# Optimization experiments

Hardware: AMD Instinct MI355X
Metric: run time of the kernel (lower is better)

## Reference

```python
import jax, jax.numpy as jnp
import numpy as np

EPS = 1e-10
BLOCK = 8


def _block_rfft2(x):
    # x: (N, 1, H, W) -> real/imag coeffs (N, K, 8, 5), matching torch.rfft(signal_ndim=2)/b**2
    N, C, H, W = x.shape
    b = BLOCK
    Hb, Wb = H // b, W // b
    # non-overlapping 8x8 blocks, row-major over (Hb, Wb) like nn.Unfold with stride=blocksize
    blocks = x[:, 0].reshape(N, Hb, b, Wb, b).transpose(0, 1, 3, 2, 4).reshape(N, Hb * Wb, b, b)
    c = jnp.fft.rfft2(blocks) / (b * b)  # (N, K, 8, 5) complex
    return jnp.real(c).astype(x.dtype), jnp.imag(c).astype(x.dtype)


def _soft_combine(a, b):
    # softmax-weighted blend of a and b along a virtual last axis (factor=1)
    stacked = jnp.stack([a, b], axis=-1)
    f = jax.nn.softmax(stacked, axis=-1)
    return a * f[..., 0] + b * f[..., 1]


def setup_inputs() -> dict:
    key = jax.random.key(0)
    k1, k2 = jax.random.split(key)
    N, H, W = 64, 512, 512
    inp = {
        "input": jax.random.normal(k1, (N, 1, H, W), dtype=jnp.float32),
        "target": jax.random.normal(k2, (N, 1, H, W), dtype=jnp.float32),
        # learned parameters at their init values (weight_size = (8, 5))
        "t_tild": jnp.zeros((BLOCK, BLOCK // 2 + 1), dtype=jnp.float32),
        "alpha": jnp.float32(0.1),
        "w_tild": jnp.float32(np.log(0.2 / 0.8)),
        "beta": jnp.float32(1.0),
        "w_phase_tild": jnp.zeros((BLOCK, BLOCK // 2 + 1), dtype=jnp.float32) - 2.0,
    }
    return inp


def reference(input, target, t_tild, alpha, w_tild, beta, w_phase_tild):
    # blockwise 2D rFFT of both images
    c0r, c0i = _block_rfft2(target)  # (N, K, 8, 5)
    c1r, c1i = _block_rfft2(input)

    # amplitude: frobenius norm over (real, imag) after +EPS, as in torch.norm(c0+EPS, dim=4)
    c0_amp = jnp.sqrt((c0r + EPS) ** 2 + (c0i + EPS) ** 2)
    c1_amp = jnp.sqrt((c1r + EPS) ** 2 + (c1i + EPS) ** 2)

    avg_lum = jnp.mean(c0_amp[:, :, 0, 0])
    t = jnp.exp(t_tild)  # (8, 5)
    lum = ((c0_amp[:, :, 0, 0] + EPS) / (avg_lum + EPS)) ** alpha  # (N, K)
    t_l = t[None, None, :, :] * lum[:, :, None, None]  # (N, K, 8, 5)

    w = jax.nn.sigmoid(w_tild)
    s = _soft_combine(t_l, (jnp.abs(c0_amp) + EPS) ** w * t_l ** (1 - w))

    # Watson amplitude distance (dropout in eval mode = identity)
    watson = (jnp.abs((c0_amp - c1_amp) / s) + EPS) ** beta + EPS
    watson = jnp.sum(watson, axis=(1, 2, 3)) ** (1.0 / beta)  # (N,)

    # phase distance
    c0_phase = jnp.arctan2(c0i, c0r + EPS)
    c1_phase = jnp.arctan2(c1i, c1r + EPS)
    w_phase = jnp.exp(w_phase_tild)  # trainable=True branch: no corner zeroing
    phase_dist = jnp.arccos(jnp.cos(c0_phase - c1_phase) * (1 - EPS * 1e3)) * w_phase
    phase_dist = jnp.sum(phase_dist, axis=(1, 2, 3))  # (N,)

    return watson + phase_dist  # reduction='none' -> (N,)
```

## Files before the change

kernel.cpp:

```cpp
#include <hip/hip_runtime.h>
#include <math.h>

#define EPSf 1e-10f
#define IMG_N 64
#define IMG_H 512
#define IMG_W 512
#define KBLK 4096
#define TOTAL_BLK (IMG_N * KBLK)
#define WG 256
#define NWG (TOTAL_BLK / WG)
#define NWG2 (TOTAL_BLK * 2 / WG)
#define CHUNKS 32

#define KCc 0.70710678118654752440f
#define SCc (1.0f / 64.0f)
#define LOG2E 1.44269504088896340736f

#define FSQRT(x) __builtin_amdgcn_sqrtf(x)
#define FRCP(x)  __builtin_amdgcn_rcpf(x)

__device__ __forceinline__ float dpp_xor1(float x) {
    int i = __builtin_bit_cast(int, x);
    i = __builtin_amdgcn_mov_dpp(i, 0xB1, 0xF, 0xF, true);
    return __builtin_bit_cast(float, i);
}

__device__ __forceinline__ float wave_red(float v) {
#pragma unroll
    for (int o = 32; o > 0; o >>= 1) v += __shfl_down(v, o, 64);
    return v;
}

__global__ __launch_bounds__(WG) void kA(const float* __restrict__ tgt,
                                         float* __restrict__ partA) {
    int gid = blockIdx.x * WG + threadIdx.x;
    int n = gid >> 12;
    int k = gid & 4095;
    int bi = k >> 6, bj = k & 63;
    const float* p = tgt + (size_t)n * (IMG_H * IMG_W) + (size_t)(bi * 8) * IMG_W + bj * 8;
    float s = 0.f;
#pragma unroll
    for (int r = 0; r < 8; r++) {
        float4 a = *(const float4*)(p + (size_t)r * IMG_W);
        float4 b = *(const float4*)(p + (size_t)r * IMG_W + 4);
        s += ((a.x + a.y) + (a.z + a.w)) + ((b.x + b.y) + (b.z + b.w));
    }
    float dc = s * (1.0f / 64.0f);
    float amp = sqrtf((dc + EPSf) * (dc + EPSf) + EPSf * EPSf);
    float wv = wave_red(amp);
    __shared__ float red[4];
    if ((threadIdx.x & 63) == 0) red[threadIdx.x >> 6] = wv;
    __syncthreads();
    if (threadIdx.x == 0) partA[blockIdx.x] = (red[0] + red[1]) + (red[2] + red[3]);
}

__global__ __launch_bounds__(1024) void kB(const float* __restrict__ partA,
                                           float* __restrict__ avgOut) {
    float v = partA[threadIdx.x];
    float wv = wave_red(v);
    __shared__ float red[16];
    if ((threadIdx.x & 63) == 0) red[threadIdx.x >> 6] = wv;
    __syncthreads();
    if (threadIdx.x == 0) {
        float s = 0.f;
#pragma unroll
        for (int i = 0; i < 16; i++) s += red[i];
        avgOut[0] = s * (1.0f / (float)TOTAL_BLK);
    }
}

#define ROWFFT(A, B, P) do { \
    float s02 = (A).x + (B).x, d02 = (A).x - (B).x; \
    float s26 = (A).z + (B).z, d26 = (A).z - (B).z; \
    float s13 = (A).y + (B).y, d13 = (A).y - (B).y; \
    float s37 = (A).w + (B).w, d37 = (A).w - (B).w; \
    float e0 = s02 + s26, e2 = s02 - s26; \
    float o0 = s13 + s37, o2 = s13 - s37; \
    float cp = KCc * (d13 - d37), cm = KCc * (d13 + d37); \
    P##_0 = SCc * (e0 + o0);  P##_1 = SCc * (d02 + cp); \
    P##_2 = SCc * (-d26 - cm); P##_3 = SCc * e2; \
    P##_4 = SCc * (-o2);      P##_5 = SCc * (d02 - cp); \
    P##_6 = SCc * (d26 - cm); P##_7 = SCc * (e0 - o0); \
} while (0)

#define DECL8(P) float P##_0, P##_1, P##_2, P##_3, P##_4, P##_5, P##_6, P##_7

#define LOADROW(ptr, r, P) do { \
    float4 A = *(const float4*)((ptr) + (size_t)(r) * IMG_W); \
    float4 B = *(const float4*)((ptr) + (size_t)(r) * IMG_W + 4); \
    ROWFFT(A, B, P); \
} while (0)

#define CFFT8M(PFX, x0r,x0i,x1r,x1i,x2r,x2i,x3r,x3i,x4r,x4i,x5r,x5i,x6r,x6i,x7r,x7i) \
    float PFX##0r, PFX##0i, PFX##1r, PFX##1i, PFX##2r, PFX##2i, PFX##3r, PFX##3i, \
          PFX##4r, PFX##4i, PFX##5r, PFX##5i, PFX##6r, PFX##6i, PFX##7r, PFX##7i; \
    { \
        float t0r = (x0r) + (x4r), t0i = (x0i) + (x4i); \
        float t1r = (x0r) - (x4r), t1i = (x0i) - (x4i); \
        float t2r = (x2r) + (x6r), t2i = (x2i) + (x6i); \
        float t3r = (x2r) - (x6r), t3i = (x2i) - (x6i); \
        float E0r = t0r + t2r, E0i = t0i + t2i; \
        float E2r = t0r - t2r, E2i = t0i - t2i; \
        float E1r = t1r + t3i, E1i = t1i - t3r; \
        float E3r = t1r - t3i, E3i = t1i + t3r; \
        float u0r = (x1r) + (x5r), u0i = (x1i) + (x5i); \
        float u1r = (x1r) - (x5r), u1i = (x1i) - (x5i); \
        float u2r = (x3r) + (x7r), u2i = (x3i) + (x7i); \
        float u3r = (x3r) - (x7r), u3i = (x3i) - (x7i); \
        float O0r = u0r + u2r, O0i = u0i + u2i; \
        float O2r = u0r - u2r, O2i = u0i - u2i; \
        float O1r = u1r + u3i, O1i = u1i - u3r; \
        float O3r = u1r - u3i, O3i = u1i + u3r; \
        float W1r = KCc * (O1r + O1i), W1i = KCc * (O1i - O1r); \
        float W2r = O2i,               W2i = -O2r; \
        float W3r = KCc * (O3i - O3r), W3i = -KCc * (O3r + O3i); \
        PFX##0r = E0r + O0r; PFX##0i = E0i + O0i; \
        PFX##1r = E1r + W1r; PFX##1i = E1i + W1i; \
        PFX##2r = E2r + W2r; PFX##2i = E2i + W2i; \
        PFX##3r = E3r + W3r; PFX##3i = E3i + W3i; \
        PFX##4r = E0r - O0r; PFX##4i = E0i - O0i; \
        PFX##5r = E1r - W1r; PFX##5i = E1i - W1i; \
        PFX##6r = E2r - W2r; PFX##6i = E2i - W2i; \
        PFX##7r = E3r - W3r; PFX##7i = E3i - W3i; \
    }

__device__ __attribute__((noinline)) float2
coef2f(float oR, float oI, float rR, float rI,
       float tq, float lq, float pq,
       float lum, float omw_llum, float w, float beta,
       int img, int b1i) {
    float oRe = oR + EPSf, oIe = oI + EPSf;
    float rRe = rR + EPSf, rIe = rI + EPSf;
    float aO = FSQRT(fmaf(oRe, oRe, oIe * oIe));
    float aR = FSQRT(fmaf(rRe, rRe, rIe * rIe));
    float a0 = img ? aR : aO;
    float dx = fabsf(aO - aR);
    float l0 = __log2f(a0 + EPSf);
    float bb = exp2f(fmaf(w, l0, lq + omw_llum));
    float t_l = tq * lum;
    float e = __expf(bb - t_l);
    float x = dx * (1.f + e) * FRCP(fmaf(bb, e, t_l));
    float dw = b1i ? x : (__powf(x + EPSf, beta) + EPSf);
    float dot = fmaf(oRe, rRe, oI * rI);
    float cosd = dot * FRCP(fmaxf(aO * aR, 1e-30f)) * (1.f - 1e-7f);
    cosd = fminf(fmaxf(cosd, -1.f), 1.f);
    float t = fabsf(cosd);
    float r = FSQRT(1.f - t);
    float pl = fmaf(fmaf(fmaf(-0.0187293f, t, 0.0742610f), t, -0.2121144f), t, 1.5707288f);
    float ac = r * pl;
    ac = (cosd < 0.f) ? (3.14159265358979f - ac) : ac;
    return make_float2(dw, ac * pq);
}

#define PAIRC(Q, LOr, LOi, HIr, HIi) do { \
    float sdr = img ? (LOr) : (HIr), sdi = img ? (LOi) : (HIi); \
    float rcr = dpp_xor1(sdr), rci = dpp_xor1(sdi); \
    float owr = img ? (HIr) : (LOr), owi = img ? (HIi) : (LOi); \
    float2 dwp = coef2f(owr, owi, rcr, rci, (Q).x, (Q).y, (Q).z, \
                        lum, omw_llum, w, beta, img, b1i); \
    sumW += dwp.x; sumP += dwp.y; \
} while (0)

#define PREFQ(V) \
    float4 q0 = tab4[base20 + 0 * 5 + (V)]; \
    float4 q1 = tab4[base20 + 1 * 5 + (V)]; \
    float4 q2 = tab4[base20 + 2 * 5 + (V)]; \
    float4 q3 = tab4[base20 + 3 * 5 + (V)];

#define COEFS2() do { \
    PAIRC(q0, X0r, X0i, X4r, X4i); \
    PAIRC(q1, X1r, X1i, X5r, X5i); \
    PAIRC(q2, X2r, X2i, X6r, X6i); \
    PAIRC(q3, X3r, X3i, X7r, X7i); \
} while (0)

__global__ __launch_bounds__(WG, 4) void kC(const float* __restrict__ tgt,
                                            const float* __restrict__ inp,
                                            const float* __restrict__ t_tild,
                                            const float* __restrict__ alphaP,
                                            const float* __restrict__ wtP,
                                            const float* __restrict__ betaP,
                                            const float* __restrict__ wptP,
                                            const float* __restrict__ avgP,
                                            float* __restrict__ partW,
                                            float* __restrict__ partP) {
    __shared__ float4 tab4[40];
    float w = 1.f / (1.f + __expf(-wtP[0]));
    if (threadIdx.x < 40) {
        float tt = t_tild[threadIdx.x];
        tab4[threadIdx.x] = make_float4(__expf(tt), (1.f - w) * tt * LOG2E,
                                        __expf(wptP[threadIdx.x]), 0.f);
    }
    __syncthreads();
    float alpha = alphaP[0];
    float beta = betaP[0];
    float avg = avgP[0];
    float lavg = __log2f(avg + EPSf);
    int b1i = (beta == 1.0f) ? 1 : 0;

    int gid = blockIdx.x * WG + threadIdx.x;
    int p = gid >> 1;
    int img = gid & 1;
    int base20 = img * 20;
    int n = p >> 12, k = p & 4095;
    int bi = k >> 6, bj = k & 63;
    size_t off = (size_t)n * (IMG_H * IMG_W) + (size_t)(bi * 8) * IMG_W + bj * 8;
    const float* src = (img ? inp : tgt) + off;

    DECL8(t0); DECL8(t1); DECL8(t2); DECL8(t3);
    DECL8(t4); DECL8(t5); DECL8(t6); DECL8(t7);
    LOADROW(src, 0, t0); LOADROW(src, 1, t1); LOADROW(src, 2, t2); LOADROW(src, 3, t3);
    LOADROW(src, 4, t4); LOADROW(src, 5, t5); LOADROW(src, 6, t6); LOADROW(src, 7, t7);

    float sumW = 0.f, sumP = 0.f;
    float lum = 0.f, omw_llum = 0.f;

    {
        PREFQ(0)
        CFFT8M(X, t0_0, 0.f, t1_0, 0.f, t2_0, 0.f, t3_0, 0.f,
                  t4_0, 0.f, t5_0, 0.f, t6_0, 0.f, t7_0, 0.f)
        float rr = X0r + EPSf, ii = X0i + EPSf;
        float myamp = FSQRT(fmaf(rr, rr, ii * ii));
        float oamp = dpp_xor1(myamp);
        float amp00 = img ? oamp : myamp;
        float llum = alpha * (__log2f(amp00 + EPSf) - lavg);
        lum = exp2f(llum);
        omw_llum = (1.f - w) * llum;
        COEFS2();
    }
    {
        PREFQ(1)
        CFFT8M(X, t0_1, t0_2, t1_1, t1_2, t2_1, t2_2, t3_1, t3_2,
                  t4_1, t4_2, t5_1, t5_2, t6_1, t6_2, t7_1, t7_2)
        COEFS2();
    }
    {
        PREFQ(2)
        CFFT8M(X, t0_3, t0_4, t1_3, t1_4, t2_3, t2_4, t3_3, t3_4,
                  t4_3, t4_4, t5_3, t5_4, t6_3, t6_4, t7_3, t7_4)
        COEFS2();
    }
    {
        PREFQ(3)
        CFFT8M(X, t0_5, t0_6, t1_5, t1_6, t2_5, t2_6, t3_5, t3_6,
                  t4_5, t4_6, t5_5, t5_6, t6_5, t6_6, t7_5, t7_6)
        COEFS2();
    }
    {
        PREFQ(4)
        CFFT8M(X, t0_7, 0.f, t1_7, 0.f, t2_7, 0.f, t3_7, 0.f,
                  t4_7, 0.f, t5_7, 0.f, t6_7, 0.f, t7_7, 0.f)
        COEFS2();
    }

    if (b1i) sumW += 20.f * 2.f * EPSf;

    float wW = wave_red(sumW);
    float wP = wave_red(sumP);
    __shared__ float redW[4], redP[4];
    if ((threadIdx.x & 63) == 0) { redW[threadIdx.x >> 6] = wW; redP[threadIdx.x >> 6] = wP; }
    __syncthreads();
    if (threadIdx.x == 0) {
        partW[blockIdx.x] = (redW[0] + redW[1]) + (redW[2] + redW[3]);
        partP[blockIdx.x] = (redP[0] + redP[1]) + (redP[2] + redP[3]);
    }
}

__global__ __launch_bounds__(64) void kD(const float* __restrict__ partW,
                                         const float* __restrict__ partP,
                                         const float* __restrict__ betaP,
                                         float* __restrict__ out) {
    int n = threadIdx.x;
    float sW = 0.f, sP = 0.f;
#pragma unroll
    for (int c = 0; c < CHUNKS; c++) {
        sW += partW[n * CHUNKS + c];
        sP += partP[n * CHUNKS + c];
    }
    float beta = betaP[0];
    float wat = (beta == 1.0f) ? sW : __powf(sW, 1.0f / beta);
    out[n] = wat + sP;
}

extern "C" void kernel_launch(void* const* d_in, const int* in_sizes, int n_in,
                              void* d_out, int out_size, void* d_ws, size_t ws_size,
                              hipStream_t stream) {
    const float* inp    = (const float*)d_in[0];
    const float* tgt    = (const float*)d_in[1];
    const float* t_tild = (const float*)d_in[2];
    const float* alphaP = (const float*)d_in[3];
    const float* wtP    = (const float*)d_in[4];
    const float* betaP  = (const float*)d_in[5];
    const float* wptP   = (const float*)d_in[6];
    float* out = (float*)d_out;
    float* ws = (float*)d_ws;
    float* partA = ws;
    float* avgV  = ws + 1024;
    float* partW = ws + 1056;
    float* partP = ws + 3104;

    hipLaunchKernelGGL(kA, dim3(NWG), dim3(WG), 0, stream, tgt, partA);
    hipLaunchKernelGGL(kB, dim3(1), dim3(1024), 0, stream, partA, avgV);
    hipLaunchKernelGGL(kC, dim3(NWG2), dim3(WG), 0, stream, tgt, inp, t_tild,
                       alphaP, wtP, betaP, wptP, avgV, partW, partP);
    hipLaunchKernelGGL(kD, dim3(1), dim3(64), 0, stream, partW, partP, betaP, out);
}
```

Measured before the change: 49.31 us.

## Fold average-luminance reduction into main kernel and batch coefficient pairs per call

Removes the single-workgroup kB launch. Each kC workgroup now re-reduces the 1024 kA partial sums itself to get the average DC amplitude, which trades a kernel launch and its dependency gap for redundant small reads in every workgroup. Separately, the noinline per-coefficient helper now processes two coefficient pairs per call. This halves call overhead and gives the compiler more independent transcendental work to interleave, at the cost of higher register pressure.

```diff
diff --git a/kernel.cpp b/kernel.cpp
--- a/kernel.cpp
+++ b/kernel.cpp
@@ -52,21 +52,6 @@
     if ((threadIdx.x & 63) == 0) red[threadIdx.x >> 6] = wv;
     __syncthreads();
     if (threadIdx.x == 0) partA[blockIdx.x] = (red[0] + red[1]) + (red[2] + red[3]);
-}
-
-__global__ __launch_bounds__(1024) void kB(const float* __restrict__ partA,
-                                           float* __restrict__ avgOut) {
-    float v = partA[threadIdx.x];
-    float wv = wave_red(v);
-    __shared__ float red[16];
-    if ((threadIdx.x & 63) == 0) red[threadIdx.x >> 6] = wv;
-    __syncthreads();
-    if (threadIdx.x == 0) {
-        float s = 0.f;
-#pragma unroll
-        for (int i = 0; i < 16; i++) s += red[i];
-        avgOut[0] = s * (1.0f / (float)TOTAL_BLK);
-    }
 }
 
 #define ROWFFT(A, B, P) do { \
@@ -125,39 +110,60 @@
     }
 
 __device__ __attribute__((noinline)) float2
-coef2f(float oR, float oI, float rR, float rI,
-       float tq, float lq, float pq,
-       float lum, float omw_llum, float w, float beta,
-       int img, int b1i) {
-    float oRe = oR + EPSf, oIe = oI + EPSf;
-    float rRe = rR + EPSf, rIe = rI + EPSf;
-    float aO = FSQRT(fmaf(oRe, oRe, oIe * oIe));
-    float aR = FSQRT(fmaf(rRe, rRe, rIe * rIe));
-    float a0 = img ? aR : aO;
-    float dx = fabsf(aO - aR);
-    float l0 = __log2f(a0 + EPSf);
-    float bb = exp2f(fmaf(w, l0, lq + omw_llum));
-    float t_l = tq * lum;
-    float e = __expf(bb - t_l);
-    float x = dx * (1.f + e) * FRCP(fmaf(bb, e, t_l));
-    float dw = b1i ? x : (__powf(x + EPSf, beta) + EPSf);
-    float dot = fmaf(oRe, rRe, oI * rI);
-    float cosd = dot * FRCP(fmaxf(aO * aR, 1e-30f)) * (1.f - 1e-7f);
-    cosd = fminf(fmaxf(cosd, -1.f), 1.f);
-    float t = fabsf(cosd);
-    float r = FSQRT(1.f - t);
-    float pl = fmaf(fmaf(fmaf(-0.0187293f, t, 0.0742610f), t, -0.2121144f), t, 1.5707288f);
-    float ac = r * pl;
-    ac = (cosd < 0.f) ? (3.14159265358979f - ac) : ac;
-    return make_float2(dw, ac * pq);
-}
-
-#define PAIRC(Q, LOr, LOi, HIr, HIi) do { \
-    float sdr = img ? (LOr) : (HIr), sdi = img ? (LOi) : (HIi); \
-    float rcr = dpp_xor1(sdr), rci = dpp_xor1(sdi); \
-    float owr = img ? (HIr) : (LOr), owi = img ? (HIi) : (LOi); \
-    float2 dwp = coef2f(owr, owi, rcr, rci, (Q).x, (Q).y, (Q).z, \
-                        lum, omw_llum, w, beta, img, b1i); \
+coef2x2(float oRA, float oIA, float rRA, float rIA, float tA, float lA, float pA,
+        float oRB, float oIB, float rRB, float rIB, float tB, float lB, float pB,
+        float lum, float omw_llum, float w, float beta, int img, int b1i) {
+    float oReA = oRA + EPSf, oIeA = oIA + EPSf;
+    float rReA = rRA + EPSf, rIeA = rIA + EPSf;
+    float oReB = oRB + EPSf, oIeB = oIB + EPSf;
+    float rReB = rRB + EPSf, rIeB = rIB + EPSf;
+    float aOA = FSQRT(fmaf(oReA, oReA, oIeA * oIeA));
+    float aRA = FSQRT(fmaf(rReA, rReA, rIeA * rIeA));
+    float aOB = FSQRT(fmaf(oReB, oReB, oIeB * oIeB));
+    float aRB = FSQRT(fmaf(rReB, rReB, rIeB * rIeB));
+    float a0A = img ? aRA : aOA;
+    float a0B = img ? aRB : aOB;
+    float dxA = fabsf(aOA - aRA);
+    float dxB = fabsf(aOB - aRB);
+    float l0A = __log2f(a0A + EPSf);
+    float l0B = __log2f(a0B + EPSf);
+    float bbA = exp2f(fmaf(w, l0A, lA + omw_llum));
+    float bbB = exp2f(fmaf(w, l0B, lB + omw_llum));
+    float tlA = tA * lum;
+    float tlB = tB * lum;
+    float eA = __expf(bbA - tlA);
+    float eB = __expf(bbB - tlB);
+    float xA = dxA * (1.f + eA) * FRCP(fmaf(bbA, eA, tlA));
+    float xB = dxB * (1.f + eB) * FRCP(fmaf(bbB, eB, tlB));
+    float dwA = b1i ? xA : (__powf(xA + EPSf, beta) + EPSf);
+    float dwB = b1i ? xB : (__powf(xB + EPSf, beta) + EPSf);
+    float dotA = fmaf(oReA, rReA, oIA * rIA);
+    float dotB = fmaf(oReB, rReB, oIB * rIB);
+    float cdA = dotA * FRCP(fmaxf(aOA * aRA, 1e-30f)) * (1.f - 1e-7f);
+    float cdB = dotB * FRCP(fmaxf(aOB * aRB, 1e-30f)) * (1.f - 1e-7f);
+    cdA = fminf(fmaxf(cdA, -1.f), 1.f);
+    cdB = fminf(fmaxf(cdB, -1.f), 1.f);
+    float tA2 = fabsf(cdA), tB2 = fabsf(cdB);
+    float rA2 = FSQRT(1.f - tA2), rB2 = FSQRT(1.f - tB2);
+    float plA = fmaf(fmaf(fmaf(-0.0187293f, tA2, 0.0742610f), tA2, -0.2121144f), tA2, 1.5707288f);
+    float plB = fmaf(fmaf(fmaf(-0.0187293f, tB2, 0.0742610f), tB2, -0.2121144f), tB2, 1.5707288f);
+    float acA = rA2 * plA;
+    float acB = rB2 * plB;
+    acA = (cdA < 0.f) ? (3.14159265358979f - acA) : acA;
+    acB = (cdB < 0.f) ? (3.14159265358979f - acB) : acB;
+    return make_float2(dwA + dwB, fmaf(acA, pA, acB * pB));
+}
+
+#define PAIRC2(QA, LAr, LAi, HAr, HAi, QB, LBr, LBi, HBr, HBi) do { \
+    float sAr = img ? (LAr) : (HAr), sAi = img ? (LAi) : (HAi); \
+    float rAr = dpp_xor1(sAr), rAi = dpp_xor1(sAi); \
+    float oAr = img ? (HAr) : (LAr), oAi = img ? (HAi) : (LAi); \
+    float sBr = img ? (LBr) : (HBr), sBi = img ? (LBi) : (HBi); \
+    float rBr = dpp_xor1(sBr), rBi = dpp_xor1(sBi); \
+    float oBr = img ? (HBr) : (LBr), oBi = img ? (HBi) : (LBi); \
+    float2 dwp = coef2x2(oAr, oAi, rAr, rAi, (QA).x, (QA).y, (QA).z, \
+                         oBr, oBi, rBr, rBi, (QB).x, (QB).y, (QB).z, \
+                         lum, omw_llum, w, beta, img, b1i); \
     sumW += dwp.x; sumP += dwp.y; \
 } while (0)
 
@@ -168,10 +174,8 @@
     float4 q3 = tab4[base20 + 3 * 5 + (V)];
 
 #define COEFS2() do { \
-    PAIRC(q0, X0r, X0i, X4r, X4i); \
-    PAIRC(q1, X1r, X1i, X5r, X5i); \
-    PAIRC(q2, X2r, X2i, X6r, X6i); \
-    PAIRC(q3, X3r, X3i, X7r, X7i); \
+    PAIRC2(q0, X0r, X0i, X4r, X4i, q1, X1r, X1i, X5r, X5i); \
+    PAIRC2(q2, X2r, X2i, X6r, X6i, q3, X3r, X3i, X7r, X7i); \
 } while (0)
 
 __global__ __launch_bounds__(WG, 4) void kC(const float* __restrict__ tgt,
@@ -181,20 +185,27 @@
                                             const float* __restrict__ wtP,
                                             const float* __restrict__ betaP,
                                             const float* __restrict__ wptP,
-                                            const float* __restrict__ avgP,
+                                            const float* __restrict__ partA,
                                             float* __restrict__ partW,
                                             float* __restrict__ partP) {
     __shared__ float4 tab4[40];
+    __shared__ float redA[4];
     float w = 1.f / (1.f + __expf(-wtP[0]));
     if (threadIdx.x < 40) {
         float tt = t_tild[threadIdx.x];
         tab4[threadIdx.x] = make_float4(__expf(tt), (1.f - w) * tt * LOG2E,
                                         __expf(wptP[threadIdx.x]), 0.f);
     }
+    {
+        float v = partA[threadIdx.x] + partA[threadIdx.x + 256] +
+                  partA[threadIdx.x + 512] + partA[threadIdx.x + 768];
+        float wv = wave_red(v);
+        if ((threadIdx.x & 63) == 0) redA[threadIdx.x >> 6] = wv;
+    }
     __syncthreads();
+    float avg = ((redA[0] + redA[1]) + (redA[2] + redA[3])) * (1.0f / (float)TOTAL_BLK);
     float alpha = alphaP[0];
     float beta = betaP[0];
-    float avg = avgP[0];
     float lavg = __log2f(avg + EPSf);
     int b1i = (beta == 1.0f) ? 1 : 0;
 
@@ -295,13 +306,11 @@
     float* out = (float*)d_out;
     float* ws = (float*)d_ws;
     float* partA = ws;
-    float* avgV  = ws + 1024;
     float* partW = ws + 1056;
     float* partP = ws + 3104;
 
     hipLaunchKernelGGL(kA, dim3(NWG), dim3(WG), 0, stream, tgt, partA);
-    hipLaunchKernelGGL(kB, dim3(1), dim3(1024), 0, stream, partA, avgV);
     hipLaunchKernelGGL(kC, dim3(NWG2), dim3(WG), 0, stream, tgt, inp, t_tild,
-                       alphaP, wtP, betaP, wptP, avgV, partW, partP);
+                       alphaP, wtP, betaP, wptP, partA, partW, partP);
     hipLaunchKernelGGL(kD, dim3(1), dim3(64), 0, stream, partW, partP, betaP, out);
 }
```

New measurement: 45.85 us (median of 4 runs). -7.0%, faster.
